# Kernel optimization log

Hardware: AMD Instinct MI355X
Metric: run time of the kernel (lower is better)

Reference implementation:

```python
import jax, jax.numpy as jnp
import numpy as np

WORD_DIM = 300
HIDDEN = 768
B, S = 128, 256
H_DIR = HIDDEN // 2          # 384 per-direction LSTM hidden
SEMA = HIDDEN // 3 * 2       # 512
STRU = HIDDEN // 3           # 256
EPS_MT = 1.0                 # MatrixTree eps


def setup_inputs() -> dict:
    key = jax.random.key(0)
    ks = jax.random.split(key, 18)
    rn = lambda k, shp, s=1.0: jax.random.normal(k, shp, dtype=jnp.float32) * s
    s_l = 1.0 / np.sqrt(H_DIR)
    s_d = 1.0 / np.sqrt(STRU)
    return {
        'input': rn(ks[0], (B, S, WORD_DIM)),
        'mask': jnp.ones((B, S, 1), jnp.float32),
        # forward-direction LSTM (PyTorch gate order i,f,g,o)
        'w_ih_f': rn(ks[1], (4 * H_DIR, WORD_DIM), s_l),
        'w_hh_f': rn(ks[2], (4 * H_DIR, H_DIR), s_l),
        'b_f': rn(ks[3], (4 * H_DIR,), s_l),
        # backward-direction LSTM
        'w_ih_b': rn(ks[4], (4 * H_DIR, WORD_DIM), s_l),
        'w_hh_b': rn(ks[5], (4 * H_DIR, H_DIR), s_l),
        'b_b': rn(ks[6], (4 * H_DIR,), s_l),
        # structured attention params
        'w_tp': rn(ks[7], (STRU, STRU), s_d),
        'b_tp': rn(ks[8], (STRU,), s_d),
        'w_tc': rn(ks[9], (STRU, STRU), s_d),
        'b_tc': rn(ks[10], (STRU,), s_d),
        'w_a': rn(ks[11], (STRU, STRU), 0.02),  # scaled so exp(scores) stays finite
        'w_root': rn(ks[12], (1, STRU), s_d),
        'root_emb': rn(ks[13], (SEMA,)),
        'w_r': rn(ks[14], (SEMA, SEMA * 3), 1.0 / np.sqrt(3 * SEMA)),
        'b_r': rn(ks[15], (SEMA,), 1.0 / np.sqrt(3 * SEMA)),
    }


def _lstm_dir(x, w_ih, w_hh, b):
    # x: [S, B, E] -> hs: [S, B, H]
    h0 = jnp.zeros((x.shape[1], w_hh.shape[1]), x.dtype)
    def step(carry, xt):
        h, c = carry
        g = xt @ w_ih.T + h @ w_hh.T + b
        i, f, gg, o = jnp.split(g, 4, axis=-1)
        c = jax.nn.sigmoid(f) * c + jax.nn.sigmoid(i) * jnp.tanh(gg)
        h = jax.nn.sigmoid(o) * jnp.tanh(c)
        return (h, c), h
    _, hs = jax.lax.scan(step, (h0, h0), x)
    return hs


def _matrix_tree(A, r):
    # A: [B,S,S] (zero diagonal), r: [B,S,1]
    bsz, seq_len = A.shape[0], A.shape[1]
    idx = jnp.arange(seq_len)
    L = -A
    L = L.at[:, idx, idx].set(A.sum(axis=1))          # column sums on diagonal
    LL = jnp.concatenate([r[..., 0][:, None, :], L[:, 1:, :]], axis=1)
    dg = LL[:, idx, idx]
    LL = LL.at[:, idx, idx].set(jnp.where(dg == 0, EPS_MT, dg))
    LL_inv = jnp.linalg.inv(LL)
    d0 = (r[..., 0] * LL_inv[:, :, 0])[:, None, :]     # [B,1,S]
    diag_inv = LL_inv[:, idx, idx]                     # [B,S]
    term1 = A * diag_inv[:, None, :]                   # A[i,j] * inv_diag[j]
    term2 = A * jnp.swapaxes(LL_inv, 1, 2)             # A[i,j] * inv[j,i]
    term1 = term1.at[:, :, 0].set(0.0)
    term2 = term2.at[:, 0, :].set(0.0)
    return d0, term1 - term2


def reference(input, mask, w_ih_f, w_hh_f, b_f, w_ih_b, w_hh_b, b_b,
              w_tp, b_tp, w_tc, b_tc, w_a, w_root, root_emb, w_r, b_r):
    bsz, seq_len = input.shape[0], input.shape[1]
    xs = jnp.swapaxes(input, 0, 1)                     # [S,B,E]
    hf = _lstm_dir(xs, w_ih_f, w_hh_f, b_f)            # [S,B,H_DIR]
    hb = _lstm_dir(xs[::-1], w_ih_b, w_hh_b, b_b)[::-1]
    out = jnp.swapaxes(jnp.concatenate([hf, hb], axis=-1), 0, 1)  # [B,S,2H]
    of_, ob = out[..., :H_DIR], out[..., H_DIR:]
    half = SEMA // 2
    vec_sema = jnp.concatenate([of_[..., :half], ob[..., :half]], axis=-1)  # [B,S,SEMA]
    vec_stru = jnp.concatenate([of_[..., half:], ob[..., half:]], axis=-1)  # [B,S,STRU]

    tp = jnp.tanh(vec_stru @ w_tp.T + b_tp)
    tc = jnp.tanh(vec_stru @ w_tc.T + b_tc)
    mask_sq = jnp.einsum('bsi,bti->bst', mask, mask)
    f = jnp.einsum('bsd,de,bte->bst', tp, w_a, tc)
    f = jnp.exp(f) * mask_sq
    f_r = jnp.exp(vec_stru @ w_root.T) * mask          # [B,S,1]
    idx = jnp.arange(seq_len)
    f = f.at[:, idx, idx].set(0.0)

    a0, a = _matrix_tree(f, f_r)                       # [B,1,S], [B,S,S]
    a_c = a
    a_p = jnp.swapaxes(jnp.concatenate([a0, a], axis=1), 1, 2)  # [B,S,S+1]

    root_embs = jnp.broadcast_to(root_emb, (bsz, 1, SEMA))
    vec_sem_root = jnp.concatenate([root_embs, vec_sema], axis=1)  # [B,S+1,SEMA]
    c = a_c @ vec_sema                                  # [B,S,SEMA]
    p = a_p @ vec_sem_root                              # [B,S,SEMA]
    output = jnp.tanh(jnp.concatenate([vec_sema, p, c], axis=-1) @ w_r.T + b_r)
    output = output * mask
    emb = output.max(axis=1)                            # [B,SEMA]
    return emb, output
```

## Files before the change

### kernel.cpp

```cpp
#include <hip/hip_runtime.h>
#include <hip/hip_fp16.h>
#include <math.h>

#define B_    128
#define S_    256
#define WORD_ 300
#define HD_   384
#define M_    32768
#define STRU_ 256
#define SEMA_ 512
#define SEG   16777216L

typedef __half half_t;
typedef _Float16 f16x8 __attribute__((ext_vector_type(8)));
typedef float    f32x4 __attribute__((ext_vector_type(4)));

template<bool BNN>
__global__ __launch_bounds__(256)
void mgemm(const half_t* __restrict__ Ag, const half_t* __restrict__ Bg,
           half_t* __restrict__ Cg,
           int M, int N, int K, int lda, int ldb, int ldc,
           long sA, long sB, long sC,
           const float* __restrict__ bias, int act,
           const float* __restrict__ d0v, const float* __restrict__ rootv)
{
    __shared__ __half As[128][40];
    __shared__ __half Bs[64][40];
    const int bz = blockIdx.z;
    const half_t* A  = Ag + (long)bz * sA;
    const half_t* Bp = Bg + (long)bz * sB;
    const int m0 = blockIdx.y * 128, n0 = blockIdx.x * 64;
    const int tid = threadIdx.x;
    const int l = tid & 63, w = tid >> 6;
    const int wm = w & 1, wn = w >> 1;
    const int lr = l & 15, lq = l >> 4;

    f32x4 acc[4][2] = {};

    for (int k0 = 0; k0 < K; k0 += 32) {
        #pragma unroll
        for (int i = 0; i < 2; i++) {
            int ch = tid + i * 256;
            int r = ch >> 2, j = ch & 3;
            *(float4*)&As[r][j * 8] = *(const float4*)(A + (long)(m0 + r) * lda + k0 + j * 8);
        }
        if (!BNN) {
            int r = tid >> 2, j = tid & 3;
            *(float4*)&Bs[r][j * 8] = *(const float4*)(Bp + (long)(n0 + r) * ldb + k0 + j * 8);
        } else {
            int k = tid & 31, nc = tid >> 5;
            float4 v = *(const float4*)(Bp + (long)(k0 + k) * ldb + n0 + nc * 8);
            const __half* hv = (const __half*)&v;
            #pragma unroll
            for (int jj = 0; jj < 8; jj++) Bs[nc * 8 + jj][k] = hv[jj];
        }
        __syncthreads();

        f16x8 af[4], bf[2];
        #pragma unroll
        for (int mf = 0; mf < 4; mf++)
            af[mf] = *(const f16x8*)&As[wm * 64 + mf * 16 + lr][lq * 8];
        #pragma unroll
        for (int nf = 0; nf < 2; nf++)
            bf[nf] = *(const f16x8*)&Bs[wn * 32 + nf * 16 + lr][lq * 8];
        #pragma unroll
        for (int mf = 0; mf < 4; mf++)
            #pragma unroll
            for (int nf = 0; nf < 2; nf++)
                acc[mf][nf] = __builtin_amdgcn_mfma_f32_16x16x32_f16(af[mf], bf[nf], acc[mf][nf], 0, 0, 0);
        __syncthreads();
    }

    #pragma unroll
    for (int mf = 0; mf < 4; mf++) {
        #pragma unroll
        for (int nf = 0; nf < 2; nf++) {
            #pragma unroll
            for (int j = 0; j < 4; j++) {
                int m = m0 + wm * 64 + mf * 16 + lq * 4 + j;
                int n = n0 + wn * 32 + nf * 16 + lr;
                float v = acc[mf][nf][j];
                if (bias) v += bias[n];
                if (d0v)  v += d0v[(long)bz * M + m] * rootv[n];
                if (act == 1)      v = tanhf(v);
                else if (act == 2) v = (m == n) ? 0.f : expf(v);
                Cg[(long)bz * sC + (long)m * ldc + n] = __float2half(v);
            }
        }
    }
}

__global__ __launch_bounds__(256)
void mgemm_final(const half_t* __restrict__ A0, const half_t* __restrict__ A1,
                 const half_t* __restrict__ A2, const half_t* __restrict__ Bw,
                 float* __restrict__ Cout, const float* __restrict__ bias,
                 const float* __restrict__ maskp)
{
    __shared__ __half As[128][40];
    __shared__ __half Bs[64][40];
    const int m0 = blockIdx.y * 128, n0 = blockIdx.x * 64;
    const int tid = threadIdx.x;
    const int l = tid & 63, w = tid >> 6;
    const int wm = w & 1, wn = w >> 1;
    const int lr = l & 15, lq = l >> 4;

    f32x4 acc[4][2] = {};

    for (int k0 = 0; k0 < 1536; k0 += 32) {
        const half_t* A = (k0 < 512) ? A0 : (k0 < 1024) ? A1 : A2;
        const int kk = k0 & 511;
        #pragma unroll
        for (int i = 0; i < 2; i++) {
            int ch = tid + i * 256;
            int r = ch >> 2, j = ch & 3;
            *(float4*)&As[r][j * 8] = *(const float4*)(A + (long)(m0 + r) * 512 + kk + j * 8);
        }
        {
            int r = tid >> 2, j = tid & 3;
            *(float4*)&Bs[r][j * 8] = *(const float4*)(Bw + (long)(n0 + r) * 1536 + k0 + j * 8);
        }
        __syncthreads();
        f16x8 af[4], bf[2];
        #pragma unroll
        for (int mf = 0; mf < 4; mf++)
            af[mf] = *(const f16x8*)&As[wm * 64 + mf * 16 + lr][lq * 8];
        #pragma unroll
        for (int nf = 0; nf < 2; nf++)
            bf[nf] = *(const f16x8*)&Bs[wn * 32 + nf * 16 + lr][lq * 8];
        #pragma unroll
        for (int mf = 0; mf < 4; mf++)
            #pragma unroll
            for (int nf = 0; nf < 2; nf++)
                acc[mf][nf] = __builtin_amdgcn_mfma_f32_16x16x32_f16(af[mf], bf[nf], acc[mf][nf], 0, 0, 0);
        __syncthreads();
    }

    #pragma unroll
    for (int mf = 0; mf < 4; mf++) {
        #pragma unroll
        for (int nf = 0; nf < 2; nf++) {
            #pragma unroll
            for (int j = 0; j < 4; j++) {
                int m = m0 + wm * 64 + mf * 16 + lq * 4 + j;
                int n = n0 + wn * 32 + nf * 16 + lr;
                float v = tanhf(acc[mf][nf][j] + bias[n]) * maskp[m];
                Cout[(long)m * 512 + n] = v;
            }
        }
    }
}

__global__ __launch_bounds__(256)
void ggemm(const float* __restrict__ x, const half_t* __restrict__ Wp,
           const float* __restrict__ bp, half_t* __restrict__ G, int chunk)
{
    __shared__ __half As[128][40];
    __shared__ __half Bs[128][40];
    const int d = blockIdx.z;
    const int ts = blockIdx.y;
    const int m0 = blockIdx.x * 128;
    const int t_orig = d ? (255 - (chunk * 128 + ts)) : (chunk * 128 + ts);
    const int tid = threadIdx.x;
    const int l = tid & 63, w = tid >> 6;
    const int wm = w & 1, wn = w >> 1;
    const int lr = l & 15, lq = l >> 4;

    f32x4 acc[4][4] = {};

    for (int k0 = 0; k0 < 320; k0 += 32) {
        #pragma unroll
        for (int i = 0; i < 2; i++) {
            int e = tid + i * 256;
            int r = e >> 2, j = (e & 3) * 8;
            *(float4*)&As[r][j] = *(const float4*)(Wp + ((long)d * 1536 + m0 + r) * 320 + k0 + j);
        }
        #pragma unroll
        for (int i = 0; i < 2; i++) {
            int e = tid + i * 256;
            int r = e >> 2, j = (e & 3) * 8;
            int k = k0 + j;
            int ka = (k + 4 <= 300) ? k : 0;
            int kb = (k + 8 <= 300) ? k + 4 : 0;
            const float* xp = x + ((long)r * 256 + t_orig) * 300;
            float4 va = *(const float4*)(xp + ka);
            float4 vb = *(const float4*)(xp + kb);
            __half* q = &Bs[r][j];
            q[0] = __float2half(va.x); q[1] = __float2half(va.y);
            q[2] = __float2half(va.z); q[3] = __float2half(va.w);
            q[4] = __float2half(vb.x); q[5] = __float2half(vb.y);
            q[6] = __float2half(vb.z); q[7] = __float2half(vb.w);
        }
        __syncthreads();
        f16x8 af[4], bf[4];
        #pragma unroll
        for (int gf = 0; gf < 4; gf++)
            af[gf] = *(const f16x8*)&As[wm * 64 + gf * 16 + lr][lq * 8];
        #pragma unroll
        for (int bi = 0; bi < 4; bi++)
            bf[bi] = *(const f16x8*)&Bs[wn * 64 + bi * 16 + lr][lq * 8];
        #pragma unroll
        for (int gf = 0; gf < 4; gf++)
            #pragma unroll
            for (int bi = 0; bi < 4; bi++)
                acc[gf][bi] = __builtin_amdgcn_mfma_f32_16x16x32_f16(af[gf], bf[bi], acc[gf][bi], 0, 0, 0);
        __syncthreads();
    }

    half_t* Gt = G + (long)(ts * 2 + d) * 196608;
    #pragma unroll
    for (int gf = 0; gf < 4; gf++) {
        #pragma unroll
        for (int bi = 0; bi < 4; bi++) {
            int g = m0 + wm * 64 + gf * 16 + lq * 4;
            int b = wn * 64 + bi * 16 + lr;
            union { __half h[4]; float2 f; } u;
            #pragma unroll
            for (int j = 0; j < 4; j++)
                u.h[j] = __float2half(acc[gf][bi][j] + bp[d * 1536 + g + j]);
            *(float2*)(Gt + ((long)(g >> 2) * 128 + b) * 4) = u.f;
        }
    }
}

__global__ __launch_bounds__(256)
void lstm_scan(const half_t* __restrict__ G, const half_t* __restrict__ Whh,
               half_t* __restrict__ Hbuf, float* __restrict__ Cst,
               half_t* __restrict__ vs, half_t* __restrict__ vst,
               unsigned* __restrict__ flags, int chunk)
{
    __shared__ __half Wl[64 * 392];
    __shared__ __half hlo[16][68];

    const int bid = blockIdx.x;
    const int d = bid / 48, rem = bid % 48;
    const int ntile = rem >> 1, btile = rem & 1;
    const int grp = d * 2 + btile;
    const int tid = threadIdx.x;
    const int l = tid & 63, w = tid >> 6;
    const int wm = w & 1, wn = w >> 1;
    const int lr = l & 15, lq = l >> 4;

    {
        const half_t* src = Whh + ((long)d * 1536 + ntile * 64) * 384;
        for (int e = tid; e < 3072; e += 256) {
            int r = e / 48, c = (e % 48) * 8;
            *(float4*)&Wl[r * 392 + c] = *(const float4*)(src + (long)r * 384 + c);
        }
    }
    float creg[4];
    if (chunk == 0) {
        creg[0] = creg[1] = creg[2] = creg[3] = 0.f;
    } else {
        #pragma unroll
        for (int i = 0; i < 4; i++) creg[i] = Cst[((long)bid * 256 + tid) * 4 + i];
    }

    const int bg0 = btile * 64 + wn * 32 + lr;
    long goff[4];
    #pragma unroll
    for (int gf = 0; gf < 2; gf++)
        #pragma unroll
        for (int bf2 = 0; bf2 < 2; bf2++) {
            const int hdg = ntile * 16 + wm * 8 + gf * 4 + lq;
            const int bg  = bg0 + bf2 * 16;
            goff[gf * 2 + bf2] = ((long)hdg * 128 + bg) * 4;
        }
    float2 gc0, gc1, gc2, gc3;
    {
        const half_t* gp0 = G + (long)(0 * 2 + d) * 196608;
        gc0 = *(const float2*)(gp0 + goff[0]);
        gc1 = *(const float2*)(gp0 + goff[1]);
        gc2 = *(const float2*)(gp0 + goff[2]);
        gc3 = *(const float2*)(gp0 + goff[3]);
    }
    __syncthreads();

    union U16 { unsigned long long u[2]; f16x8 v; };

    for (int s = 0; s < 128; ++s) {
        const int gstep = chunk * 128 + s;
        const int p = gstep & 1;
        const half_t* hin = Hbuf + (long)(p * 2 + d) * 128 * 384;

        float2 gn0, gn1, gn2, gn3;
        {
            const int sn = (s < 127) ? s + 1 : 127;
            const half_t* gpn = G + (long)(sn * 2 + d) * 196608;
            gn0 = *(const float2*)(gpn + goff[0]);
            gn1 = *(const float2*)(gpn + goff[1]);
            gn2 = *(const float2*)(gpn + goff[2]);
            gn3 = *(const float2*)(gpn + goff[3]);
        }

        f16x8 hb[12][2];
        #pragma unroll
        for (int it = 0; it < 12; ++it)
            #pragma unroll
            for (int bf2 = 0; bf2 < 2; bf2++) {
                const unsigned long long* hp = (const unsigned long long*)
                    (hin + (long)(bg0 + bf2 * 16) * 384 + it * 32 + lq * 8);
                U16 t;
                t.u[0] = __hip_atomic_load(hp,     __ATOMIC_RELAXED, __HIP_MEMORY_SCOPE_AGENT);
                t.u[1] = __hip_atomic_load(hp + 1, __ATOMIC_RELAXED, __HIP_MEMORY_SCOPE_AGENT);
                hb[it][bf2] = t.v;
            }

        f32x4 acc[2][2] = {};
        #pragma unroll
        for (int it = 0; it < 12; ++it) {
            f16x8 af[2];
            #pragma unroll
            for (int gf = 0; gf < 2; gf++)
                af[gf] = *(const f16x8*)&Wl[(wm * 32 + gf * 16 + lr) * 392 + it * 32 + lq * 8];
            #pragma unroll
            for (int gf = 0; gf < 2; gf++)
                #pragma unroll
                for (int bf2 = 0; bf2 < 2; bf2++)
                    acc[gf][bf2] = __builtin_amdgcn_mfma_f32_16x16x32_f16(af[gf], hb[it][bf2], acc[gf][bf2], 0, 0, 0);
        }

        #pragma unroll
        for (int gf = 0; gf < 2; gf++) {
            #pragma unroll
            for (int bf2 = 0; bf2 < 2; bf2++) {
                const int hd_l = wm * 8 + gf * 4 + lq;
                const int bl_  = wn * 32 + bf2 * 16 + lr;
                union { float2 f; __half h[4]; } gu;
                const int ci = gf * 2 + bf2;
                gu.f = (ci == 0) ? gc0 : (ci == 1) ? gc1 : (ci == 2) ? gc2 : gc3;
                float gi  = acc[gf][bf2][0] + __half2float(gu.h[0]);
                float gfo = acc[gf][bf2][1] + __half2float(gu.h[1]);
                float gg  = acc[gf][bf2][2] + __half2float(gu.h[2]);
                float go  = acc[gf][bf2][3] + __half2float(gu.h[3]);
                float c = creg[ci];
                float si = 1.f / (1.f + expf(-gi));
                float sf = 1.f / (1.f + expf(-gfo));
                float so = 1.f / (1.f + expf(-go));
                c = sf * c + si * tanhf(gg);
                creg[ci] = c;
                hlo[hd_l][bl_] = __float2half(so * tanhf(c));
            }
        }
        __syncthreads();

        f16x8 v;
        int bg_w = 0, hd0_w = 0;
        if (tid < 128) {
            const int b_l = tid & 63, h8 = tid >> 6;
            #pragma unroll
            for (int j = 0; j < 8; j++) v[j] = (_Float16)hlo[h8 * 8 + j][b_l];
            bg_w  = btile * 64 + b_l;
            hd0_w = ntile * 16 + h8 * 8;
            U16 sv; sv.v = v;
            unsigned long long* hp = (unsigned long long*)
                (Hbuf + ((long)((p ^ 1) * 2 + d) * 128 + bg_w) * 384 + hd0_w);
            __hip_atomic_store(hp,     sv.u[0], __ATOMIC_RELAXED, __HIP_MEMORY_SCOPE_AGENT);
            __hip_atomic_store(hp + 1, sv.u[1], __ATOMIC_RELAXED, __HIP_MEMORY_SCOPE_AGENT);
        }
        __syncthreads();
        if (s < 127 && tid == 0)
            __hip_atomic_store(&flags[(grp * 24 + ntile) * 16], (unsigned)(gstep + 1),
                               __ATOMIC_RELAXED, __HIP_MEMORY_SCOPE_AGENT);
        if (tid < 128) {
            const int t_orig = d ? 255 - gstep : gstep;
            const long m = (long)bg_w * 256 + t_orig;
            if (hd0_w < 256)
                __builtin_nontemporal_store(v, (f16x8*)(vs + m * 512 + d * 256 + hd0_w));
            else
                __builtin_nontemporal_store(v, (f16x8*)(vst + m * 256 + d * 128 + (hd0_w - 256)));
        }

        if (s < 127) {
            const unsigned tgt = (unsigned)(gstep + 1);
            const unsigned fidx = (grp * 24 + (l % 24)) * 16;
            while (true) {
                unsigned fv = __hip_atomic_load(&flags[fidx], __ATOMIC_RELAXED,
                                                __HIP_MEMORY_SCOPE_AGENT);
                if (__all(fv >= tgt)) break;
                __builtin_amdgcn_s_sleep(1);
            }
            asm volatile("" ::: "memory");
        }
        gc0 = gn0; gc1 = gn1; gc2 = gn2; gc3 = gn3;
    }

    #pragma unroll
    for (int i = 0; i < 4; i++) Cst[((long)bid * 256 + tid) * 4 + i] = creg[i];
}

__global__ void pack_wih(const float* __restrict__ wf, const float* __restrict__ wb,
                         const float* __restrict__ bfv, const float* __restrict__ bbv,
                         half_t* __restrict__ Wp, float* __restrict__ bp)
{
    int i = blockIdx.x * 256 + threadIdx.x;
    if (i < 983040) {
        int k = i % 320, pr = (i / 320) % 1536, d = i / 491520;
        int q = pr & 3, hd = pr >> 2;
        float v = (k < 300) ? (d ? wb : wf)[(q * 384 + hd) * 300 + k] : 0.f;
        Wp[i] = __float2half(v);
    }
    if (i < 3072) {
        int d = i / 1536, pr = i % 1536;
        int q = pr & 3, hd = pr >> 2;
        bp[i] = (d ? bbv : bfv)[q * 384 + hd];
    }
}
__global__ void pack_whh(const float* __restrict__ wf, const float* __restrict__ wb,
                         half_t* __restrict__ Wh)
{
    int i = blockIdx.x * 256 + threadIdx.x;
    if (i >= 1179648) return;
    int k = i % 384, pr = (i / 384) % 1536, d = i / 589824;
    int q = pr & 3, hd = pr >> 2;
    Wh[i] = __float2half((d ? wb : wf)[(q * 384 + hd) * 384 + k]);
}
__global__ void conv16(const float* __restrict__ s, half_t* __restrict__ d, long n)
{
    long i = (long)blockIdx.x * 256 + threadIdx.x;
    if (i < n) d[i] = __float2half(s[i]);
}
__global__ void convT16(const float* __restrict__ s, half_t* __restrict__ d, int R, int C)
{
    int i = blockIdx.x * 256 + threadIdx.x;
    if (i >= R * C) return;
    int r = i / C, c = i % C;
    d[(long)c * R + r] = __float2half(s[i]);
}

__global__ __launch_bounds__(256)
void frow_kernel(const half_t* __restrict__ vst, const float* __restrict__ wroot,
                 float* __restrict__ fr)
{
    int row  = blockIdx.x * 4 + (threadIdx.x >> 6);
    int lane = threadIdx.x & 63;
    const half_t* v = vst + (long)row * 256;
    float s = 0.f;
    for (int k = lane; k < 256; k += 64) s += __half2float(v[k]) * wroot[k];
    #pragma unroll
    for (int off = 32; off; off >>= 1) s += __shfl_down(s, off);
    if (lane == 0) fr[row] = expf(s);
}

__global__ __launch_bounds__(1024)
void invert_gj(const half_t* __restrict__ fA, const float* __restrict__ fr,
               half_t* __restrict__ LLinv)
{
    __shared__ float colbuf[2][256];
    __shared__ float rowbuf[2][256];
    __shared__ float csum[4][256];
    const int bz = blockIdx.x;
    const half_t* A = fA + (long)bz * 65536;
    const int tid = threadIdx.x;
    const int c = tid & 255, rh = tid >> 8;
    float m[64];

    float s = 0.f;
    #pragma unroll
    for (int i = 0; i < 64; i++) {
        float v = __half2float(A[(long)(rh * 64 + i) * 256 + c]);
        m[i] = v; s += v;
    }
    csum[rh][c] = s;
    __syncthreads();
    float diag = csum[0][c] + csum[1][c] + csum[2][c] + csum[3][c];
    const float frv = fr[bz * 256 + c];
    #pragma unroll
    for (int i = 0; i < 64; i++) {
        int r = rh * 64 + i;
        float v = (r == c) ? ((diag == 0.f) ? 1.f : diag) : -m[i];
        if (rh == 0 && i == 0) {
            v = frv;
            if (c == 0 && v == 0.f) v = 1.f;
        }
        m[i] = v;
    }
    __syncthreads();

    for (int k = 0; k < 256; k++) {
        const int p = k & 1;
        const int kh = k >> 6, kl = k & 63;
        if (c == k) {
            #pragma unroll
            for (int i = 0; i < 64; i++) colbuf[p][rh * 64 + i] = m[i];
        }
        if (rh == kh) {
            float pv = 0.f;
            #pragma unroll
            for (int i = 0; i < 64; i++) pv = (i == kl) ? m[i] : pv;
            rowbuf[p][c] = pv;
        }
        __syncthreads();
        const float piv  = colbuf[p][k];
        const float pinv = 1.f / piv;
        const float rv   = rowbuf[p][c] * pinv;
        if (c == k) {
            #pragma unroll
            for (int i = 0; i < 64; i++) m[i] = -colbuf[p][rh * 64 + i] * pinv;
        } else {
            #pragma unroll
            for (int i = 0; i < 64; i++) m[i] -= colbuf[p][rh * 64 + i] * rv;
        }
        if (rh == kh) {
            const float dv = (c == k) ? pinv : rv;
            #pragma unroll
            for (int i = 0; i < 64; i++) m[i] = (i == kl) ? dv : m[i];
        }
    }

    #pragma unroll
    for (int i = 0; i < 64; i++)
        LLinv[(long)bz * 65536 + (long)(rh * 64 + i) * 256 + c] = __float2half(m[i]);
}

__global__ void diag_d0_k(const half_t* __restrict__ LLinv, const float* __restrict__ fr,
                          float* __restrict__ diagv, float* __restrict__ d0)
{
    int i = blockIdx.x * 256 + threadIdx.x;
    if (i >= 32768) return;
    int b = i >> 8, s = i & 255;
    diagv[i] = __half2float(LLinv[(long)b * 65536 + s * 257]);
    d0[i]    = fr[i] * __half2float(LLinv[(long)b * 65536 + s * 256]);
}

__global__ __launch_bounds__(256)
void assemble_a(half_t* __restrict__ fA, const half_t* __restrict__ LLinv,
                const float* __restrict__ diagv, half_t* __restrict__ aT)
{
    __shared__ float  ll[32][33];
    __shared__ __half av[32][33];
    const int bz = blockIdx.z;
    const int s0 = (blockIdx.x >> 3) * 32, t0 = (blockIdx.x & 7) * 32;
    const int tid = threadIdx.x;
    const long base = (long)bz * 65536;
    #pragma unroll
    for (int it = 0; it < 4; it++) {
        int i = (tid >> 5) + it * 8, j = tid & 31;
        ll[i][j] = __half2float(LLinv[base + (long)(t0 + i) * 256 + (s0 + j)]);
    }
    __syncthreads();
    #pragma unroll
    for (int it = 0; it < 4; it++) {
        int si = (tid >> 5) + it * 8, tj = tid & 31;
        int s = s0 + si, t = t0 + tj;
        long idx = base + (long)s * 256 + t;
        float Av = __half2float(fA[idx]);
        float t1 = (t > 0) ? diagv[(bz << 8) + t] : 0.f;
        float t2 = (s > 0) ? ll[tj][si] : 0.f;
        __half hv = __float2half(Av * (t1 - t2));
        fA[idx] = hv;
        av[si][tj] = hv;
    }
    __syncthreads();
    #pragma unroll
    for (int it = 0; it < 4; it++) {
        int ti = (tid >> 5) + it * 8, sj = tid & 31;
        aT[base + (long)(t0 + ti) * 256 + (s0 + sj)] = av[sj][ti];
    }
}

__global__ __launch_bounds__(256)
void emb_max(const float* __restrict__ outp, float* __restrict__ emb)
{
    int b = blockIdx.x;
    for (int n = threadIdx.x; n < 512; n += 256) {
        const float* p = outp + (long)b * 131072 + n;
        float mx = -3.4e38f;
        for (int t = 0; t < 256; t++) mx = fmaxf(mx, p[(long)t * 512]);
        emb[b * 512 + n] = mx;
    }
}

__global__ void diag_ws(float* out, int n, float v)
{
    int i = blockIdx.x * 256 + threadIdx.x;
    if (i < n) out[i] = v;
}

extern "C" void kernel_launch(void* const* d_in, const int* in_sizes, int n_in,
                              void* d_out, int out_size, void* d_ws, size_t ws_size,
                              hipStream_t stream)
{
    const float* x     = (const float*)d_in[0];
    const float* mask  = (const float*)d_in[1];
    const float* wihf  = (const float*)d_in[2];
    const float* whhf  = (const float*)d_in[3];
    const float* bf    = (const float*)d_in[4];
    const float* wihb  = (const float*)d_in[5];
    const float* whhb  = (const float*)d_in[6];
    const float* bb    = (const float*)d_in[7];
    const float* wtp   = (const float*)d_in[8];
    const float* btp   = (const float*)d_in[9];
    const float* wtc   = (const float*)d_in[10];
    const float* btc   = (const float*)d_in[11];
    const float* wa    = (const float*)d_in[12];
    const float* wroot = (const float*)d_in[13];
    const float* remb  = (const float*)d_in[14];
    const float* wr    = (const float*)d_in[15];
    const float* br    = (const float*)d_in[16];

    if (ws_size < 134217728ULL) {
        float enc = 100.0f + (float)((double)ws_size * 1e-9);
        diag_ws<<<dim3((out_size + 255) / 256), 256, 0, stream>>>((float*)d_out, out_size, enc);
        return;
    }

    char* ws = (char*)d_ws;
    half_t* G     = (half_t*)(ws + 0);
    half_t* vs    = (half_t*)(ws + 100663296);
    half_t* tp    = (half_t*)(ws + 0 * SEG);
    half_t* tc    = (half_t*)(ws + 1 * SEG);
    half_t* tmp   = (half_t*)(ws + 2 * SEG);
    half_t* fA    = (half_t*)(ws + 3 * SEG);
    half_t* LL    = (half_t*)(ws + 4 * SEG);
    half_t* aT    = (half_t*)(ws + 5 * SEG);
    half_t* cbuf  = (half_t*)(ws + 0 * SEG);
    half_t* pbuf  = (half_t*)(ws + 2 * SEG);
    half_t* wr16  = (half_t*)(ws + 4 * SEG);

    float* ob = (float*)d_out;
    half_t*   Wp16  = (half_t*)(ob + 11000000);
    half_t*   Whh16 = (half_t*)(ob + 11491520);
    float*    bp    = ob + 12081344;
    half_t*   wtp16 = (half_t*)(ob + 12084416);
    half_t*   wtc16 = (half_t*)(ob + 12117184);
    half_t*   wa16T = (half_t*)(ob + 12149952);
    float*    fr    = ob + 12182720;
    float*    d0    = ob + 12215488;
    float*    diagv = ob + 12248256;
    float*    Cst   = ob + 12281024;
    half_t*   Hbuf  = (half_t*)(ob + 12379328);
    unsigned* flags = (unsigned*)(ob + 12500000);
    half_t*   vst   = (half_t*)(ob + 12648448);

    float* emb  = (float*)d_out;
    float* outp = (float*)d_out + 65536;

    hipMemsetAsync(Hbuf, 0, 393216, stream);
    hipMemsetAsync(flags, 0, 6144, stream);
    pack_wih<<<dim3(3840), 256, 0, stream>>>(wihf, wihb, bf, bb, Wp16, bp);
    pack_whh<<<dim3(4608), 256, 0, stream>>>(whhf, whhb, Whh16);
    conv16<<<dim3(256), 256, 0, stream>>>(wtp, wtp16, 65536);
    conv16<<<dim3(256), 256, 0, stream>>>(wtc, wtc16, 65536);
    convT16<<<dim3(256), 256, 0, stream>>>(wa, wa16T, 256, 256);

    for (int c = 0; c < 2; c++) {
        ggemm<<<dim3(12, 128, 2), 256, 0, stream>>>(x, Wp16, bp, G, c);
        lstm_scan<<<dim3(96), 256, 0, stream>>>(G, Whh16, Hbuf, Cst, vs, vst, flags, c);
    }

    frow_kernel<<<dim3(8192), 256, 0, stream>>>(vst, wroot, fr);

    mgemm<false><<<dim3(4, 256, 1), 256, 0, stream>>>(
        vst, wtp16, tp, M_, 256, 256, 256, 256, 256, 0, 0, 0, btp, 1, nullptr, nullptr);
    mgemm<false><<<dim3(4, 256, 1), 256, 0, stream>>>(
        vst, wtc16, tc, M_, 256, 256, 256, 256, 256, 0, 0, 0, btc, 1, nullptr, nullptr);

    mgemm<false><<<dim3(4, 256, 1), 256, 0, stream>>>(
        tp, wa16T, tmp, M_, 256, 256, 256, 256, 256, 0, 0, 0, nullptr, 0, nullptr, nullptr);

    mgemm<false><<<dim3(4, 2, 128), 256, 0, stream>>>(
        tmp, tc, fA, 256, 256, 256, 256, 256, 256, 65536, 65536, 65536,
        nullptr, 2, nullptr, nullptr);

    invert_gj<<<dim3(128), 1024, 0, stream>>>(fA, fr, LL);
    diag_d0_k<<<dim3(128), 256, 0, stream>>>(LL, fr, diagv, d0);
    assemble_a<<<dim3(64, 1, 128), 256, 0, stream>>>(fA, LL, diagv, aT);

    conv16<<<dim3(3072), 256, 0, stream>>>(wr, wr16, 786432);

    mgemm<true><<<dim3(8, 2, 128), 256, 0, stream>>>(
        fA, vs, cbuf, 256, 512, 256, 256, 512, 512, 65536, 131072, 131072,
        nullptr, 0, nullptr, nullptr);

    mgemm<true><<<dim3(8, 2, 128), 256, 0, stream>>>(
        aT, vs, pbuf, 256, 512, 256, 256, 512, 512, 65536, 131072, 131072,
        nullptr, 0, d0, remb);

    mgemm_final<<<dim3(8, 256, 1), 256, 0, stream>>>(vs, pbuf, cbuf, wr16, outp, br, mask);

    emb_max<<<dim3(128), 256, 0, stream>>>(outp, emb);
}
```

Baseline: 3.334 ms.

## Replace LSTM inter-block flag barrier with parity-tagged hidden-state polling

Drops the per-step flag array, the block-wide sync before publishing the flag, and the spin on flags. Instead, each 8-byte chunk of the published hidden state carries a parity bit in its lowest mantissa bit, and consumers poll the data itself until every chunk shows the expected parity. This removes a store-then-flag round trip and a barrier from the 256-step serial recurrence. In exchange, the LSB of each fp16 word in the recurrent state is overwritten, which slightly perturbs precision, and correctness relies on 8-byte atomic stores being seen whole and on the double buffer never running more than one step ahead.

```diff
diff --git a/kernel.cpp b/kernel.cpp
--- a/kernel.cpp
+++ b/kernel.cpp
@@ -225,8 +225,7 @@
 __global__ __launch_bounds__(256)
 void lstm_scan(const half_t* __restrict__ G, const half_t* __restrict__ Whh,
                half_t* __restrict__ Hbuf, float* __restrict__ Cst,
-               half_t* __restrict__ vs, half_t* __restrict__ vst,
-               unsigned* __restrict__ flags, int chunk)
+               half_t* __restrict__ vs, half_t* __restrict__ vst, int chunk)
 {
     __shared__ __half Wl[64 * 392];
     __shared__ __half hlo[16][68];
@@ -234,7 +233,6 @@
     const int bid = blockIdx.x;
     const int d = bid / 48, rem = bid % 48;
     const int ntile = rem >> 1, btile = rem & 1;
-    const int grp = d * 2 + btile;
     const int tid = threadIdx.x;
     const int l = tid & 63, w = tid >> 6;
     const int wm = w & 1, wn = w >> 1;
@@ -292,18 +290,31 @@
             gn3 = *(const float2*)(gpn + goff[3]);
         }
 
+        const unsigned long long tg = (unsigned long long)((gstep >> 1) & 1);
         f16x8 hb[12][2];
-        #pragma unroll
-        for (int it = 0; it < 12; ++it)
-            #pragma unroll
-            for (int bf2 = 0; bf2 < 2; bf2++) {
-                const unsigned long long* hp = (const unsigned long long*)
-                    (hin + (long)(bg0 + bf2 * 16) * 384 + it * 32 + lq * 8);
-                U16 t;
-                t.u[0] = __hip_atomic_load(hp,     __ATOMIC_RELAXED, __HIP_MEMORY_SCOPE_AGENT);
-                t.u[1] = __hip_atomic_load(hp + 1, __ATOMIC_RELAXED, __HIP_MEMORY_SCOPE_AGENT);
-                hb[it][bf2] = t.v;
+        unsigned need = 0x00FFFFFFu;
+        while (need) {
+            #pragma unroll
+            for (int it = 0; it < 12; ++it) {
+                #pragma unroll
+                for (int bf2 = 0; bf2 < 2; bf2++) {
+                    const unsigned bit = 1u << (it * 2 + bf2);
+                    if (need & bit) {
+                        const unsigned long long* hp = (const unsigned long long*)
+                            (hin + (long)(bg0 + bf2 * 16) * 384 + it * 32 + lq * 8);
+                        unsigned long long u0 = __hip_atomic_load(hp,     __ATOMIC_RELAXED, __HIP_MEMORY_SCOPE_AGENT);
+                        unsigned long long u1 = __hip_atomic_load(hp + 1, __ATOMIC_RELAXED, __HIP_MEMORY_SCOPE_AGENT);
+                        if ((u0 & 1ull) == tg && (u1 & 1ull) == tg) {
+                            U16 t;
+                            t.u[0] = u0 & ~1ull;
+                            t.u[1] = u1 & ~1ull;
+                            hb[it][bf2] = t.v;
+                            need &= ~bit;
+                        }
+                    }
+                }
             }
+        }
 
         f32x4 acc[2][2] = {};
         #pragma unroll
@@ -343,25 +354,21 @@
         }
         __syncthreads();
 
-        f16x8 v;
-        int bg_w = 0, hd0_w = 0;
         if (tid < 128) {
             const int b_l = tid & 63, h8 = tid >> 6;
+            f16x8 v;
             #pragma unroll
             for (int j = 0; j < 8; j++) v[j] = (_Float16)hlo[h8 * 8 + j][b_l];
-            bg_w  = btile * 64 + b_l;
-            hd0_w = ntile * 16 + h8 * 8;
+            const int bg_w  = btile * 64 + b_l;
+            const int hd0_w = ntile * 16 + h8 * 8;
             U16 sv; sv.v = v;
+            const unsigned long long wt = (unsigned long long)(((gstep + 1) >> 1) & 1);
+            sv.u[0] = (sv.u[0] & ~1ull) | wt;
+            sv.u[1] = (sv.u[1] & ~1ull) | wt;
             unsigned long long* hp = (unsigned long long*)
                 (Hbuf + ((long)((p ^ 1) * 2 + d) * 128 + bg_w) * 384 + hd0_w);
             __hip_atomic_store(hp,     sv.u[0], __ATOMIC_RELAXED, __HIP_MEMORY_SCOPE_AGENT);
             __hip_atomic_store(hp + 1, sv.u[1], __ATOMIC_RELAXED, __HIP_MEMORY_SCOPE_AGENT);
-        }
-        __syncthreads();
-        if (s < 127 && tid == 0)
-            __hip_atomic_store(&flags[(grp * 24 + ntile) * 16], (unsigned)(gstep + 1),
-                               __ATOMIC_RELAXED, __HIP_MEMORY_SCOPE_AGENT);
-        if (tid < 128) {
             const int t_orig = d ? 255 - gstep : gstep;
             const long m = (long)bg_w * 256 + t_orig;
             if (hd0_w < 256)
@@ -370,17 +377,6 @@
                 __builtin_nontemporal_store(v, (f16x8*)(vst + m * 256 + d * 128 + (hd0_w - 256)));
         }
 
-        if (s < 127) {
-            const unsigned tgt = (unsigned)(gstep + 1);
-            const unsigned fidx = (grp * 24 + (l % 24)) * 16;
-            while (true) {
-                unsigned fv = __hip_atomic_load(&flags[fidx], __ATOMIC_RELAXED,
-                                                __HIP_MEMORY_SCOPE_AGENT);
-                if (__all(fv >= tgt)) break;
-                __builtin_amdgcn_s_sleep(1);
-            }
-            asm volatile("" ::: "memory");
-        }
         gc0 = gn0; gc1 = gn1; gc2 = gn2; gc3 = gn3;
     }
 
@@ -629,14 +625,12 @@
     float*    diagv = ob + 12248256;
     float*    Cst   = ob + 12281024;
     half_t*   Hbuf  = (half_t*)(ob + 12379328);
-    unsigned* flags = (unsigned*)(ob + 12500000);
     half_t*   vst   = (half_t*)(ob + 12648448);
 
     float* emb  = (float*)d_out;
     float* outp = (float*)d_out + 65536;
 
     hipMemsetAsync(Hbuf, 0, 393216, stream);
-    hipMemsetAsync(flags, 0, 6144, stream);
     pack_wih<<<dim3(3840), 256, 0, stream>>>(wihf, wihb, bf, bb, Wp16, bp);
     pack_whh<<<dim3(4608), 256, 0, stream>>>(whhf, whhb, Whh16);
     conv16<<<dim3(256), 256, 0, stream>>>(wtp, wtp16, 65536);
@@ -645,7 +639,7 @@
 
     for (int c = 0; c < 2; c++) {
         ggemm<<<dim3(12, 128, 2), 256, 0, stream>>>(x, Wp16, bp, G, c);
-        lstm_scan<<<dim3(96), 256, 0, stream>>>(G, Whh16, Hbuf, Cst, vs, vst, flags, c);
+        lstm_scan<<<dim3(96), 256, 0, stream>>>(G, Whh16, Hbuf, Cst, vs, vst, c);
     }
 
     frow_kernel<<<dim3(8192), 256, 0, stream>>>(vst, wroot, fr);
```

Result: slower. 4.154 ms (+24.6%).
